# Kernel tuning notes

Hardware: AMD Instinct MI355X
Metric: run time of the kernel (lower is better)

Reference implementation:

```python
import jax, jax.numpy as jnp
import numpy as np
from jax import lax

B, C, H, W = 32, 128, 56, 56
SIZE = C * H * W
EPS = 1e-5
SLOPE = 0.1


def setup_inputs() -> dict:
    key = jax.random.key(0)
    ks = jax.random.split(key, 12)
    return {
        "ax": jax.random.normal(ks[0], (B, C, H, W), dtype=jnp.float32),
        "mx": jax.random.normal(ks[1], (B, C, H, W), dtype=jnp.float32),
        # grouped conv1d (groups=SIZE, k=2, no bias) == per-position pair weights [SIZE, 2]
        "cfc_w": jax.random.normal(ks[2], (SIZE, 2), dtype=jnp.float32) * 0.1,
        # BatchNorm1d (eval mode) params over SIZE channels
        "bn_gamma": jax.random.normal(ks[3], (SIZE,), dtype=jnp.float32) * 0.1 + 1.0,
        "bn_beta": jax.random.normal(ks[4], (SIZE,), dtype=jnp.float32) * 0.1,
        "bn_mean": jax.random.normal(ks[5], (SIZE,), dtype=jnp.float32) * 0.1,
        "bn_var": jax.random.uniform(ks[6], (SIZE,), dtype=jnp.float32, minval=0.5, maxval=1.5),
        # conv3x3, C->C, bias
        "conv_w": jax.random.normal(ks[7], (C, C, 3, 3), dtype=jnp.float32) * (1.0 / np.sqrt(C * 9)),
        "conv_b": jax.random.normal(ks[8], (C,), dtype=jnp.float32) * 0.01,
        # BatchNorm2d (eval mode) params over C channels
        "bn2_gamma": jax.random.normal(ks[9], (C,), dtype=jnp.float32) * 0.1 + 1.0,
        "bn2_beta": jax.random.normal(ks[10], (C,), dtype=jnp.float32) * 0.1,
        "bn2_mean": jax.random.normal(ks[11], (C,), dtype=jnp.float32) * 0.1,
        "bn2_var": jax.random.uniform(jax.random.fold_in(key, 99), (C,), dtype=jnp.float32, minval=0.5, maxval=1.5),
    }


def reference(ax, mx, cfc_w, bn_gamma, bn_beta, bn_mean, bn_var,
              conv_w, conv_b, bn2_gamma, bn2_beta, bn2_mean, bn2_var):
    b, c, h, w = ax.shape
    a = ax.reshape(b, -1)  # [B, SIZE]
    m = mx.reshape(b, -1)
    # degenerate grouped Conv1d(k=2, groups=SIZE): z_i = w_i0 * a_i + w_i1 * m_i
    z = cfc_w[:, 0] * a + cfc_w[:, 1] * m
    # BatchNorm1d (eval) + LeakyReLU(0.1)
    z = (z - bn_mean) * (bn_gamma / jnp.sqrt(bn_var + EPS)) + bn_beta
    z = jax.nn.leaky_relu(z, SLOPE).reshape(b, c, h, w)
    # conv3x3 (stride 1, pad 1) + bias
    y = lax.conv_general_dilated(z, conv_w, window_strides=(1, 1),
                                 padding=((1, 1), (1, 1)),
                                 dimension_numbers=("NCHW", "OIHW", "NCHW"))
    y = y + conv_b[None, :, None, None]
    # BatchNorm2d (eval) + LeakyReLU(0.1)
    scale = (bn2_gamma / jnp.sqrt(bn2_var + EPS))[None, :, None, None]
    y = (y - bn2_mean[None, :, None, None]) * scale + bn2_beta[None, :, None, None]
    return jax.nn.leaky_relu(y, SLOPE)
```

## Files before the change

kernel.cpp:

```cpp
#include <hip/hip_runtime.h>

#define B_ 32
#define C_ 128
#define H_ 56
#define W_ 56
#define HW_ (H_*W_)
#define SIZE_ (C_*HW_)
#define NPIX_ (B_*HW_)
#define HP_ 58
#define WP_ 58
#define PLANE_ (HP_*WP_*C_)
#define K_ 1152
#define EPS_ 1e-5f
#define SLOPE_ 0.1f

typedef __bf16 bf16x8 __attribute__((ext_vector_type(8)));
typedef float  f32x4  __attribute__((ext_vector_type(4)));

__device__ __forceinline__ ushort f2bf(float x) {
    union { float f; unsigned u; } v; v.f = x;
    return (ushort)((v.u + 0x7FFFu + ((v.u >> 16) & 1u)) >> 16);
}
__device__ __forceinline__ float lrelu(float z) { return z > 0.f ? z : SLOPE_ * z; }

__device__ __forceinline__ void glds16(const ushort* g, ushort* l) {
    __builtin_amdgcn_global_load_lds(
        (const __attribute__((address_space(1))) unsigned int*)g,
        (__attribute__((address_space(3))) unsigned int*)l, 16, 0, 0);
}

__global__ __launch_bounds__(256) void prep_kernel(
    const float* __restrict__ conv_w, const float* __restrict__ conv_b,
    const float* __restrict__ g2, const float* __restrict__ b2,
    const float* __restrict__ m2, const float* __restrict__ v2,
    const float2* __restrict__ cfc, const float* __restrict__ g1,
    const float* __restrict__ b1, const float* __restrict__ mu1,
    const float* __restrict__ v1,
    ushort* __restrict__ wA, float* __restrict__ scale2, float* __restrict__ shift2,
    float* __restrict__ p0, float* __restrict__ p1, float* __restrict__ p2)
{
    int tid = blockIdx.x * 256 + threadIdx.x;
    if (tid < C_ * K_) {
        int co = tid / K_;
        int k  = tid - co * K_;
        int khkw = k >> 7, ci = k & 127;
        int kh = khkw / 3, kw = khkw - 3 * kh;
        wA[tid] = f2bf(conv_w[((co * C_ + ci) * 3 + kh) * 3 + kw]);
    }
    if (tid < C_) {
        float sc = g2[tid] * rsqrtf(v2[tid] + EPS_);
        scale2[tid] = sc;
        shift2[tid] = (conv_b[tid] - m2[tid]) * sc + b2[tid];
    }
    if (tid < SIZE_) {
        float sc = g1[tid] * rsqrtf(v1[tid] + EPS_);
        float2 wv = cfc[tid];
        p0[tid] = wv.x * sc;
        p1[tid] = wv.y * sc;
        p2[tid] = b1[tid] - mu1[tid] * sc;
    }
}

__global__ __launch_bounds__(256) void zfuse_kernel(
    const float4* __restrict__ ax, const float4* __restrict__ mx,
    const float4* __restrict__ p0, const float4* __restrict__ p1,
    const float4* __restrict__ p2, ushort* __restrict__ zp)
{
    __shared__ ushort tile[W_ * 132];
    const int hp = blockIdx.x, b = blockIdx.y;
    const int tid = threadIdx.x;
    ushort* row = zp + (size_t)b * PLANE_ + (size_t)hp * (WP_ * C_);
    if (hp == 0 || hp == HP_ - 1) {
        uint2* r2 = (uint2*)row;
        for (int i = tid; i < WP_ * C_ / 4; i += 256) r2[i] = make_uint2(0u, 0u);
        return;
    }
    const int h = hp - 1;
    const int base4 = (b * SIZE_) >> 2;
    for (int i = tid; i < 1792; i += 256) {
        int c  = i / 14;
        int w4 = i - c * 14;
        int s4 = c * (HW_ / 4) + h * (W_ / 4) + w4;
        float4 a = ax[base4 + s4];
        float4 m = mx[base4 + s4];
        float4 q0 = p0[s4], q1 = p1[s4], q2 = p2[s4];
        int wb = w4 * 4;
        tile[(wb + 0) * 132 + c] = f2bf(lrelu(a.x * q0.x + m.x * q1.x + q2.x));
        tile[(wb + 1) * 132 + c] = f2bf(lrelu(a.y * q0.y + m.y * q1.y + q2.y));
        tile[(wb + 2) * 132 + c] = f2bf(lrelu(a.z * q0.z + m.z * q1.z + q2.z));
        tile[(wb + 3) * 132 + c] = f2bf(lrelu(a.w * q0.w + m.w * q1.w + q2.w));
    }
    __syncthreads();
    if (tid < C_) {
        row[tid] = 0;
        row[(WP_ - 1) * C_ + tid] = 0;
    }
    for (int j = tid; j < 1792; j += 256) {
        int w = j >> 5, cc = j & 31;
        *(uint2*)(row + C_ + w * C_ + cc * 4) = *(const uint2*)(tile + w * 132 + cc * 4);
    }
}

__global__ __launch_bounds__(256) void conv_kernel(
    const ushort* __restrict__ zp, const ushort* __restrict__ wA,
    const float* __restrict__ scale2, const float* __restrict__ shift2,
    float* __restrict__ out)
{
    __shared__ ushort As[128 * 32];
    __shared__ ushort Bs[128 * 32];

    const int tid  = threadIdx.x;
    const int wave = tid >> 6, lane = tid & 63;
    const int l16  = lane & 15, quad = lane >> 4;
    const int pbase = blockIdx.x * 128;

    const int srow = wave * 32 + (lane >> 2);
    const int sch  = lane & 3;
    const ushort* agA = wA + srow * K_ + sch * 8;

    int pf0 = pbase + srow;
    int bb0 = pf0 / HW_, pi0 = pf0 - bb0 * HW_;
    int h0 = pi0 / W_, w0 = pi0 - h0 * W_;
    const ushort* bgB0 = zp + (size_t)bb0 * PLANE_ + (h0 * WP_ + w0) * C_ + sch * 8;
    int pf1 = pf0 + 16;
    int bb1 = pf1 / HW_, pi1 = pf1 - bb1 * HW_;
    int h1 = pi1 / W_, w1 = pi1 - h1 * W_;
    const ushort* bgB1 = zp + (size_t)bb1 * PLANE_ + (h1 * WP_ + w1) * C_ + sch * 8;

    ushort* lA0 = As + (wave * 32) * 32;
    ushort* lA1 = As + (wave * 32 + 16) * 32;
    ushort* lB0 = Bs + (wave * 32) * 32;
    ushort* lB1 = Bs + (wave * 32 + 16) * 32;

    const int cob = (wave & 1) * 64;
    const int pxb = (wave >> 1) * 64;

    f32x4 acc[4][4] = {};

    for (int tap = 0; tap < 9; ++tap) {
        const int kh = tap / 3, kw = tap - kh * 3;
        const int zoff = (kh * WP_ + kw) * C_;
        const int aoff = tap * C_;
        #pragma unroll
        for (int ks = 0; ks < 4; ++ks) {
            const int ko = ks * 32;
            __syncthreads();
            glds16(agA + aoff + ko,            lA0);
            glds16(agA + 16 * K_ + aoff + ko,  lA1);
            glds16(bgB0 + zoff + ko,           lB0);
            glds16(bgB1 + zoff + ko,           lB1);
            __syncthreads();
            bf16x8 af[4], bfr[4];
            #pragma unroll
            for (int mt = 0; mt < 4; ++mt)
                af[mt] = *(const bf16x8*)(As + (cob + mt * 16 + l16) * 32 + quad * 8);
            #pragma unroll
            for (int nt = 0; nt < 4; ++nt)
                bfr[nt] = *(const bf16x8*)(Bs + (pxb + nt * 16 + l16) * 32 + quad * 8);
            #pragma unroll
            for (int mt = 0; mt < 4; ++mt)
                #pragma unroll
                for (int nt = 0; nt < 4; ++nt)
                    acc[mt][nt] = __builtin_amdgcn_mfma_f32_16x16x32_bf16(
                        af[mt], bfr[nt], acc[mt][nt], 0, 0, 0);
        }
    }

    int pob[4];
    #pragma unroll
    for (int nt = 0; nt < 4; ++nt) {
        int pf = pbase + pxb + nt * 16 + l16;
        int bb = pf / HW_;
        pob[nt] = bb * SIZE_ + (pf - bb * HW_);
    }
    #pragma unroll
    for (int mt = 0; mt < 4; ++mt) {
        #pragma unroll
        for (int r = 0; r < 4; ++r) {
            int co = cob + mt * 16 + quad * 4 + r;
            float sc = scale2[co], sh = shift2[co];
            #pragma unroll
            for (int nt = 0; nt < 4; ++nt) {
                float v = acc[mt][nt][r] * sc + sh;
                out[(size_t)pob[nt] + co * HW_] = lrelu(v);
            }
        }
    }
}

extern "C" void kernel_launch(void* const* d_in, const int* in_sizes, int n_in,
                              void* d_out, int out_size, void* d_ws, size_t ws_size,
                              hipStream_t stream) {
    const float* ax     = (const float*)d_in[0];
    const float* mx     = (const float*)d_in[1];
    const float* cfc    = (const float*)d_in[2];
    const float* bn_g   = (const float*)d_in[3];
    const float* bn_b   = (const float*)d_in[4];
    const float* bn_m   = (const float*)d_in[5];
    const float* bn_v   = (const float*)d_in[6];
    const float* conv_w = (const float*)d_in[7];
    const float* conv_b = (const float*)d_in[8];
    const float* g2     = (const float*)d_in[9];
    const float* b2     = (const float*)d_in[10];
    const float* m2     = (const float*)d_in[11];
    const float* v2     = (const float*)d_in[12];
    float* out = (float*)d_out;

    char* ws = (char*)d_ws;
    ushort* zp     = (ushort*)ws;
    ushort* wA     = (ushort*)(ws + 27557888);
    float*  scale2 = (float*)(ws + 27852800);
    float*  shift2 = (float*)(ws + 27853312);
    float*  p0     = (float*)(ws + 27853824);
    float*  p1     = (float*)(ws + 29459456);
    float*  p2     = (float*)(ws + 31065088);

    prep_kernel<<<dim3((SIZE_ + 255) / 256), 256, 0, stream>>>(
        conv_w, conv_b, g2, b2, m2, v2, (const float2*)cfc,
        bn_g, bn_b, bn_m, bn_v, wA, scale2, shift2, p0, p1, p2);
    zfuse_kernel<<<dim3(HP_, B_), 256, 0, stream>>>(
        (const float4*)ax, (const float4*)mx,
        (const float4*)p0, (const float4*)p1, (const float4*)p2, zp);
    conv_kernel<<<dim3(NPIX_ / 128), 256, 0, stream>>>(zp, wA, scale2, shift2, out);
}
```

Measured before the change: 238.3 us.

## Double-buffer conv LDS tiles and XOR-swizzle chunk layout

Gives the implicit-GEMM conv kernel two LDS buffers, so the global-to-LDS load of the next K-slice is issued before the MFMAs on the current slice run, and cuts two barriers per step to one. It also XOR-swizzles the 16-byte chunk index by row on both the store and the fragment reads to reduce LDS bank conflicts. The cost is double the LDS footprint, which may lower occupancy, and the correctness of the prefetch now depends on the loads being complete when the single barrier is reached.

Measured after the change: 237.3 us. Within noise of the previous version (-0.4%).

```diff
diff --git a/kernel.cpp b/kernel.cpp
--- a/kernel.cpp
+++ b/kernel.cpp
@@ -106,8 +106,8 @@
     const float* __restrict__ scale2, const float* __restrict__ shift2,
     float* __restrict__ out)
 {
-    __shared__ ushort As[128 * 32];
-    __shared__ ushort Bs[128 * 32];
+    __shared__ ushort As[2][128 * 32];
+    __shared__ ushort Bs[2][128 * 32];
 
     const int tid  = threadIdx.x;
     const int wave = tid >> 6, lane = tid & 63;
@@ -115,7 +115,8 @@
     const int pbase = blockIdx.x * 128;
 
     const int srow = wave * 32 + (lane >> 2);
-    const int sch  = lane & 3;
+    const int skey = (srow >> 1) & 3;
+    const int sch  = (lane & 3) ^ skey;
     const ushort* agA = wA + srow * K_ + sch * 8;
 
     int pf0 = pbase + srow;
@@ -127,44 +128,56 @@
     int h1 = pi1 / W_, w1 = pi1 - h1 * W_;
     const ushort* bgB1 = zp + (size_t)bb1 * PLANE_ + (h1 * WP_ + w1) * C_ + sch * 8;
 
-    ushort* lA0 = As + (wave * 32) * 32;
-    ushort* lA1 = As + (wave * 32 + 16) * 32;
-    ushort* lB0 = Bs + (wave * 32) * 32;
-    ushort* lB1 = Bs + (wave * 32 + 16) * 32;
+    const int lofs0 = (wave * 32) * 32;
+    const int lofs1 = (wave * 32 + 16) * 32;
 
     const int cob = (wave & 1) * 64;
     const int pxb = (wave >> 1) * 64;
+    const int rquad = quad ^ ((l16 >> 1) & 3);
 
     f32x4 acc[4][4] = {};
 
+#define STAGE(buf, aoff, boff)                                    \
+    do {                                                          \
+        glds16(agA + (aoff),           As[buf] + lofs0);          \
+        glds16(agA + 16 * K_ + (aoff), As[buf] + lofs1);          \
+        glds16(bgB0 + (boff),          Bs[buf] + lofs0);          \
+        glds16(bgB1 + (boff),          Bs[buf] + lofs1);          \
+    } while (0)
+
+    STAGE(0, 0, 0);
+    __syncthreads();
+
+    int zoff = 0, kw = 0;
     for (int tap = 0; tap < 9; ++tap) {
-        const int kh = tap / 3, kw = tap - kh * 3;
-        const int zoff = (kh * WP_ + kw) * C_;
-        const int aoff = tap * C_;
+        const int znext = (kw == 2) ? zoff + (WP_ - 2) * C_ : zoff + C_;
         #pragma unroll
         for (int ks = 0; ks < 4; ++ks) {
-            const int ko = ks * 32;
-            __syncthreads();
-            glds16(agA + aoff + ko,            lA0);
-            glds16(agA + 16 * K_ + aoff + ko,  lA1);
-            glds16(bgB0 + zoff + ko,           lB0);
-            glds16(bgB1 + zoff + ko,           lB1);
-            __syncthreads();
+            const int buf  = ks & 1;
+            const int step = tap * 4 + ks;
+            if (step < 35) {
+                const int boffn = (ks < 3) ? zoff + (ks + 1) * 32 : znext;
+                STAGE(buf ^ 1, (step + 1) * 32, boffn);
+            }
             bf16x8 af[4], bfr[4];
             #pragma unroll
             for (int mt = 0; mt < 4; ++mt)
-                af[mt] = *(const bf16x8*)(As + (cob + mt * 16 + l16) * 32 + quad * 8);
+                af[mt] = *(const bf16x8*)(As[buf] + (cob + mt * 16 + l16) * 32 + rquad * 8);
             #pragma unroll
             for (int nt = 0; nt < 4; ++nt)
-                bfr[nt] = *(const bf16x8*)(Bs + (pxb + nt * 16 + l16) * 32 + quad * 8);
+                bfr[nt] = *(const bf16x8*)(Bs[buf] + (pxb + nt * 16 + l16) * 32 + rquad * 8);
             #pragma unroll
             for (int mt = 0; mt < 4; ++mt)
                 #pragma unroll
                 for (int nt = 0; nt < 4; ++nt)
                     acc[mt][nt] = __builtin_amdgcn_mfma_f32_16x16x32_bf16(
                         af[mt], bfr[nt], acc[mt][nt], 0, 0, 0);
+            __syncthreads();
         }
-    }
+        zoff = znext;
+        if (kw == 2) kw = 0; else ++kw;
+    }
+#undef STAGE
 
     int pob[4];
     #pragma unroll
```
